# Performance work log

Hardware: AMD Instinct MI355X
Metric: run time of the kernel (lower is better)

The kernel has to match this reference:

```python
import jax, jax.numpy as jnp
import numpy as np

B, N, E, K = 4, 50000, 160000, 1000
C, L = 128, 3


def setup_inputs() -> dict:
    key = jax.random.key(0)
    ks = jax.random.split(key, 16)
    x = jax.random.normal(ks[0], (B, N, 1), jnp.float32)
    edges = jax.random.randint(ks[1], (B, 2, E), 0, N)
    defense_indices = jax.random.randint(ks[2], (B, K), 0, N)
    # GIN layer MLPs: layer l is Linear(in,C) -> ReLU -> Linear(C,C); layer 0 in=1
    w1_first = jax.random.normal(ks[3], (1, C), jnp.float32) * (1.0 / np.sqrt(1))
    w1_rest = jax.random.normal(ks[4], (L - 1, C, C), jnp.float32) * (1.0 / np.sqrt(C))
    w2 = jax.random.normal(ks[5], (L, C, C), jnp.float32) * (1.0 / np.sqrt(C))
    b1 = jax.random.normal(ks[6], (L, C), jnp.float32) * 0.02
    b2 = jax.random.normal(ks[7], (L, C), jnp.float32) * 0.02
    pol_w = jax.random.normal(ks[8], (C, 1), jnp.float32) * (1.0 / np.sqrt(C))
    pol_b = jax.random.normal(ks[9], (1,), jnp.float32) * 0.02
    val_w = jax.random.normal(ks[10], (C, 1), jnp.float32) * (1.0 / np.sqrt(C))
    val_b = jax.random.normal(ks[11], (1,), jnp.float32) * 0.02
    return {"x": x, "edges": edges, "defense_indices": defense_indices,
            "nop_index": 0, "w1_first": w1_first, "w1_rest": w1_rest,
            "w2": w2, "b1": b1, "b2": b2, "pol_w": pol_w, "pol_b": pol_b,
            "val_w": val_w, "val_b": val_b}


def reference(x, edges, defense_indices, nop_index, w1_first, w1_rest, w2, b1, b2, pol_w, pol_b, val_w, val_b):
    def gin_layer(h, src, dst, w1_l, b1_l, w2_l, b2_l):
        # sum-aggregate neighbor features (source_to_target), eps = 0
        agg = jax.ops.segment_sum(h[src], dst, num_segments=N)
        z = h + agg
        return jnp.maximum(z @ w1_l + b1_l, 0.0) @ w2_l + b2_l

    def per_graph(xg, eg):
        src, dst = eg[0], eg[1]
        h = gin_layer(xg, src, dst, w1_first, b1[0], w2[0], b2[0])
        for l in range(1, L):
            h = jnp.maximum(h, 0.0)  # inter-layer activation
            h = gin_layer(h, src, dst, w1_rest[l - 1], b1[l], w2[l], b2[l])
        return h

    emb = jax.vmap(per_graph)(x, edges)       # [B, N, C]
    emb = jnp.maximum(emb, 0.0)               # self.activation after GIN
    def_emb = jax.vmap(lambda e, i: e[i])(emb, defense_indices)  # [B, K, C]
    wait = def_emb[:, nop_index, :]           # [B, C]
    policy = jnp.squeeze(def_emb @ pol_w + pol_b, -1)  # [B, K]
    value = jnp.squeeze(wait @ val_w + val_b)          # [B]
    return (policy, value)
```

## Files before the change

### kernel.cpp

```cpp
#include <hip/hip_runtime.h>
#include <hip/hip_bf16.h>

#define BB 4
#define NN 50000
#define EE 160000
#define KK 1000
#define CH 128
#define TM 64
#define NTILES ((NN + TM - 1) / TM)
#define TILES_TOTAL (BB * NTILES)
#define SCAN_CHUNK 2048
#define SCAN_NB ((NN + SCAN_CHUNK - 1) / SCAN_CHUNK)

typedef unsigned short u16;
typedef unsigned int u32;
typedef __attribute__((ext_vector_type(8))) short short8;
typedef __attribute__((ext_vector_type(4))) float f32x4;

__device__ __forceinline__ int ZIDX(int m, int k) {
  return (m << 7) | (k ^ ((m & 7) << 3));
}

__device__ __forceinline__ u16 f2b(float f) {
  __hip_bfloat16 h = __float2bfloat16(f);
  return *reinterpret_cast<u16*>(&h);
}
__device__ __forceinline__ float b2f(u32 lo16) {
  return __uint_as_float(lo16 << 16);
}

__global__ __launch_bounds__(256)
void prep_all(const float* __restrict__ w1r, const float* __restrict__ w2,
              u16* __restrict__ img, int* __restrict__ cnt) {
  int stride = gridDim.x * blockDim.x;
  int gtid = blockIdx.x * blockDim.x + threadIdx.x;
  for (int i = gtid; i < BB * NN; i += stride) cnt[i] = 0;
  for (int f = gtid; f < 5 * CH * CH; f += stride) {
    int e = f & 7;
    int lane = (f >> 3) & 63;
    int ks = (f >> 9) & 3;
    int ct = (f >> 11) & 1;
    int wv = (f >> 12) & 3;
    int mat = f >> 14;
    int n = wv * 32 + ct * 16 + (lane & 15);
    int k = ks * 32 + (lane >> 4) * 8 + e;
    const float* src;
    switch (mat) {
      case 0: src = w2; break;
      case 1: src = w1r; break;
      case 2: src = w2 + 16384; break;
      case 3: src = w1r + 16384; break;
      default: src = w2 + 32768; break;
    }
    img[f] = f2b(src[(k << 7) + n]);
  }
}

__global__ __launch_bounds__(256)
void csr_count(const int* __restrict__ edges, int* __restrict__ cnt) {
  int stride = gridDim.x * blockDim.x;
  for (int i = blockIdx.x * blockDim.x + threadIdx.x; i < BB * EE; i += stride) {
    int b = i / EE, e = i - b * EE;
    int dst = edges[(b * 2 + 1) * EE + e];
    atomicAdd(&cnt[b * NN + dst], 1);
  }
}

__global__ __launch_bounds__(256)
void scan_local(const int* __restrict__ cnt, int* __restrict__ offs,
                int* __restrict__ bsum) {
  __shared__ int sdata[256];
  const int g = blockIdx.y, blk = blockIdx.x, t = threadIdx.x;
  const int i0 = blk * SCAN_CHUNK + t * 8;
  int v[8];
  int s = 0;
#pragma unroll
  for (int j = 0; j < 8; ++j) {
    int i = i0 + j;
    v[j] = (i < NN) ? cnt[g * NN + i] : 0;
    s += v[j];
  }
  sdata[t] = s;
  __syncthreads();
#pragma unroll
  for (int off = 1; off < 256; off <<= 1) {
    int vv = (t >= off) ? sdata[t - off] : 0;
    __syncthreads();
    sdata[t] += vv;
    __syncthreads();
  }
  int run = sdata[t] - s;
#pragma unroll
  for (int j = 0; j < 8; ++j) {
    int i = i0 + j;
    if (i < NN) offs[g * (NN + 1) + i] = run;
    run += v[j];
  }
  if (t == 255) bsum[g * SCAN_NB + blk] = sdata[255];
}

__global__ __launch_bounds__(256)
void scan_add(int* __restrict__ offs, int* __restrict__ woff,
              const int* __restrict__ bsum) {
  const int g = blockIdx.y, blk = blockIdx.x, t = threadIdx.x;
  int boff = 0;
  for (int j = 0; j < blk; ++j) boff += bsum[g * SCAN_NB + j];
  const int i0 = blk * SCAN_CHUNK + t * 8;
#pragma unroll
  for (int j = 0; j < 8; ++j) {
    int i = i0 + j;
    if (i < NN) {
      int val = offs[g * (NN + 1) + i] + boff;
      offs[g * (NN + 1) + i] = val;
      woff[g * NN + i] = val;
    }
  }
  if (blk == SCAN_NB - 1 && t == 255)
    offs[g * (NN + 1) + NN] = boff + bsum[g * SCAN_NB + blk];
}

__global__ __launch_bounds__(256)
void csr_fill(const int* __restrict__ edges, int* __restrict__ woff,
              int* __restrict__ csr) {
  int stride = gridDim.x * blockDim.x;
  for (int i = blockIdx.x * blockDim.x + threadIdx.x; i < BB * EE; i += stride) {
    int b = i / EE, e = i - b * EE;
    int src = edges[(b * 2) * EE + e];
    int dst = edges[(b * 2 + 1) * EE + e];
    int pos = atomicAdd(&woff[b * NN + dst], 1);
    csr[b * EE + pos] = (src << 6) | (dst & 63);
  }
}

template <bool L0>
__global__ __launch_bounds__(256, 4)
void gin_layer(const void* __restrict__ hin_v, u16* __restrict__ hout,
               const int* __restrict__ offs, const int* __restrict__ csr,
               const float* __restrict__ w1f,
               const u16* __restrict__ imgf_w1,
               const u16* __restrict__ imgf_w2,
               const float* __restrict__ b1v, const float* __restrict__ b2v) {
  __shared__ u16 zt[TM * CH];
  __shared__ float part[TM * 4];

  const int tid = threadIdx.x;
  const int lane = tid & 63;
  const int wv = tid >> 6;
  const int lr = lane & 15;
  const int g = lane >> 4;
  const int cb = wv * 32;

  const int wg = blockIdx.x;
  const int tile = (wg & 7) * (TILES_TOTAL / 8) + (wg >> 3);
  const int b = tile / NTILES;
  const int t0 = (tile % NTILES) * TM;
  const int nm = min(TM, NN - t0);

  const int m = tid >> 2;
  const int p = tid & 3;

  if (L0) {
    const float* x = (const float*)hin_v;
    int start = 0, end = 0;
    if (m < nm) {
      start = offs[b * (NN + 1) + t0 + m];
      end = offs[b * (NN + 1) + t0 + m + 1];
    }
    float s = 0.f;
    if (m < nm) {
      if (p == 0) s = x[b * NN + t0 + m];
      for (int e = start + p; e < end; e += 4)
        s += x[b * NN + (((u32)csr[b * EE + e]) >> 6)];
    }
    part[(m << 2) + p] = s;
    __syncthreads();
    float z0 = part[m << 2] + part[(m << 2) + 1] + part[(m << 2) + 2] +
               part[(m << 2) + 3];
#pragma unroll
    for (int jj = 0; jj < 4; ++jj) {
      int c0 = (p << 5) + (jj << 3);
      short8 tv;
#pragma unroll
      for (int t = 0; t < 8; ++t)
        tv[t] = (short)f2b(fmaxf(z0 * w1f[c0 + t] + b1v[c0 + t], 0.f));
      *(short8*)&zt[ZIDX(m, c0)] = tv;
    }
    __syncthreads();
  } else {
    const u16* h = (const u16*)hin_v;
    int start = 0, end = 0;
    if (m < nm) {
      start = offs[b * (NN + 1) + t0 + m];
      end = offs[b * (NN + 1) + t0 + m + 1];
    }
    float acc[32];
    if (m < nm) {
      const uint4* hr =
          (const uint4*)(h + ((size_t)(b * NN + t0 + m) << 7)) + (p << 2);
#pragma unroll
      for (int j = 0; j < 4; ++j) {
        uint4 v = hr[j];
        acc[j*8+0] = b2f(v.x & 0xffff); acc[j*8+1] = b2f(v.x >> 16);
        acc[j*8+2] = b2f(v.y & 0xffff); acc[j*8+3] = b2f(v.y >> 16);
        acc[j*8+4] = b2f(v.z & 0xffff); acc[j*8+5] = b2f(v.z >> 16);
        acc[j*8+6] = b2f(v.w & 0xffff); acc[j*8+7] = b2f(v.w >> 16);
      }
      for (int e = start; e < end; ++e) {
        int src = ((u32)csr[b * EE + e]) >> 6;
        const uint4* sr =
            (const uint4*)(h + ((size_t)(b * NN + src) << 7)) + (p << 2);
#pragma unroll
        for (int j = 0; j < 4; ++j) {
          uint4 v = sr[j];
          acc[j*8+0] += b2f(v.x & 0xffff); acc[j*8+1] += b2f(v.x >> 16);
          acc[j*8+2] += b2f(v.y & 0xffff); acc[j*8+3] += b2f(v.y >> 16);
          acc[j*8+4] += b2f(v.z & 0xffff); acc[j*8+5] += b2f(v.z >> 16);
          acc[j*8+6] += b2f(v.w & 0xffff); acc[j*8+7] += b2f(v.w >> 16);
        }
      }
    } else {
#pragma unroll
      for (int t = 0; t < 32; ++t) acc[t] = 0.f;
    }
#pragma unroll
    for (int jj = 0; jj < 4; ++jj) {
      int c0 = (p << 5) + (jj << 3);
      short8 tv;
#pragma unroll
      for (int t = 0; t < 8; ++t) tv[t] = (short)f2b(acc[(jj << 3) + t]);
      *(short8*)&zt[ZIDX(m, c0)] = tv;
    }
    __syncthreads();

    short8 fw1[2][4];
#pragma unroll
    for (int ct = 0; ct < 2; ++ct)
#pragma unroll
      for (int ks = 0; ks < 4; ++ks)
        fw1[ct][ks] = *(const short8*)
            &imgf_w1[(((((wv << 1) | ct) << 2) | ks) << 9) + (lane << 3)];
    f32x4 a1[4][2];
#pragma unroll
    for (int rt = 0; rt < 4; ++rt)
#pragma unroll
      for (int ct = 0; ct < 2; ++ct) a1[rt][ct] = (f32x4){0.f, 0.f, 0.f, 0.f};
#pragma unroll
    for (int ks = 0; ks < 4; ++ks) {
      int kb = (ks << 5) + (g << 3);
      short8 af[4];
#pragma unroll
      for (int rt = 0; rt < 4; ++rt)
        af[rt] = *(const short8*)&zt[ZIDX((rt << 4) + lr, kb)];
#pragma unroll
      for (int rt = 0; rt < 4; ++rt)
#pragma unroll
        for (int ct = 0; ct < 2; ++ct)
          a1[rt][ct] = __builtin_amdgcn_mfma_f32_16x16x32_bf16(
              af[rt], fw1[ct][ks], a1[rt][ct], 0, 0, 0);
    }
    __syncthreads();

#pragma unroll
    for (int rt = 0; rt < 4; ++rt)
#pragma unroll
      for (int ct = 0; ct < 2; ++ct) {
        int col = cb + (ct << 4) + lr;
        float bias = b1v[col];
#pragma unroll
        for (int r = 0; r < 4; ++r) {
          int row = (rt << 4) + (g << 2) + r;
          zt[ZIDX(row, col)] = f2b(fmaxf(a1[rt][ct][r] + bias, 0.f));
        }
      }
    __syncthreads();
  }

  short8 fw2[2][4];
#pragma unroll
  for (int ct = 0; ct < 2; ++ct)
#pragma unroll
    for (int ks = 0; ks < 4; ++ks)
      fw2[ct][ks] = *(const short8*)
          &imgf_w2[(((((wv << 1) | ct) << 2) | ks) << 9) + (lane << 3)];
  f32x4 a2[4][2];
#pragma unroll
  for (int rt = 0; rt < 4; ++rt)
#pragma unroll
    for (int ct = 0; ct < 2; ++ct) a2[rt][ct] = (f32x4){0.f, 0.f, 0.f, 0.f};
#pragma unroll
  for (int ks = 0; ks < 4; ++ks) {
    int kb = (ks << 5) + (g << 3);
    short8 af[4];
#pragma unroll
    for (int rt = 0; rt < 4; ++rt)
      af[rt] = *(const short8*)&zt[ZIDX((rt << 4) + lr, kb)];
#pragma unroll
    for (int rt = 0; rt < 4; ++rt)
#pragma unroll
      for (int ct = 0; ct < 2; ++ct)
        a2[rt][ct] = __builtin_amdgcn_mfma_f32_16x16x32_bf16(
            af[rt], fw2[ct][ks], a2[rt][ct], 0, 0, 0);
  }
  __syncthreads();

#pragma unroll
  for (int rt = 0; rt < 4; ++rt)
#pragma unroll
    for (int ct = 0; ct < 2; ++ct) {
      int col = cb + (ct << 4) + lr;
      float bias = b2v[col];
#pragma unroll
      for (int r = 0; r < 4; ++r) {
        int row = (rt << 4) + (g << 2) + r;
        zt[ZIDX(row, col)] = f2b(fmaxf(a2[rt][ct][r] + bias, 0.f));
      }
    }
  __syncthreads();

  for (int i = tid; i < 1024; i += 256) {
    int mm = i >> 4, c0 = (i & 15) << 3;
    if (mm < nm) {
      uint4 v = *(const uint4*)&zt[ZIDX(mm, c0)];
      *(uint4*)&hout[(((size_t)(b * NN + t0 + mm)) << 7) + c0] = v;
    }
  }
}

__global__ __launch_bounds__(256)
void heads_kernel(const u16* __restrict__ emb, const int* __restrict__ didx,
                  const int* __restrict__ nopp, const float* __restrict__ pol_w,
                  const float* __restrict__ pol_b, const float* __restrict__ val_w,
                  const float* __restrict__ val_b, float* __restrict__ out) {
  int gw = (blockIdx.x * blockDim.x + threadIdx.x) >> 6;
  int lane = threadIdx.x & 63;
  if (gw >= BB * KK) return;
  int b = gw / KK, k = gw - b * KK;
  int node = didx[b * KK + k];
  const u16* e = emb + (((size_t)(b * NN + node)) << 7);
  u32 v = *(const u32*)&e[lane << 1];
  float f0 = __uint_as_float(v << 16);
  float f1 = __uint_as_float(v & 0xffff0000u);
  float s = f0 * pol_w[lane << 1] + f1 * pol_w[(lane << 1) + 1];
#pragma unroll
  for (int off = 32; off; off >>= 1) s += __shfl_down(s, off);
  if (lane == 0) out[b * KK + k] = s + pol_b[0];
  if (k == nopp[0]) {
    float vv = f0 * val_w[lane << 1] + f1 * val_w[(lane << 1) + 1];
#pragma unroll
    for (int off = 32; off; off >>= 1) vv += __shfl_down(vv, off);
    if (lane == 0) out[BB * KK + b] = vv + val_b[0];
  }
}

extern "C" void kernel_launch(void* const* d_in, const int* in_sizes, int n_in,
                              void* d_out, int out_size, void* d_ws, size_t ws_size,
                              hipStream_t stream) {
  const float* x     = (const float*)d_in[0];
  const int*   edges = (const int*)d_in[1];
  const int*   didx  = (const int*)d_in[2];
  const int*   nopp  = (const int*)d_in[3];
  const float* w1f   = (const float*)d_in[4];
  const float* w1r   = (const float*)d_in[5];
  const float* w2    = (const float*)d_in[6];
  const float* b1    = (const float*)d_in[7];
  const float* b2    = (const float*)d_in[8];
  const float* pol_w = (const float*)d_in[9];
  const float* pol_b = (const float*)d_in[10];
  const float* val_w = (const float*)d_in[11];
  const float* val_b = (const float*)d_in[12];
  float* out = (float*)d_out;

  char* ws = (char*)d_ws;
  u16* hA = (u16*)ws;            ws += (size_t)BB * NN * CH * 2;
  u16* hB = (u16*)ws;            ws += (size_t)BB * NN * CH * 2;
  u16* img = (u16*)ws;           ws += (size_t)5 * CH * CH * 2;
  int* offs = (int*)ws;          ws += (size_t)BB * (NN + 1) * 4;
  int* woff = (int*)ws;          ws += (size_t)BB * NN * 4;
  int* cnt  = (int*)ws;          ws += (size_t)BB * NN * 4;
  int* bsum = (int*)ws;          ws += (size_t)BB * SCAN_NB * 4;
  int* csr  = (int*)ws;          ws += (size_t)BB * EE * 4;

  prep_all<<<784, 256, 0, stream>>>(w1r, w2, img, cnt);
  csr_count<<<1250, 256, 0, stream>>>(edges, cnt);
  scan_local<<<dim3(SCAN_NB, BB), 256, 0, stream>>>(cnt, offs, bsum);
  scan_add<<<dim3(SCAN_NB, BB), 256, 0, stream>>>(offs, woff, bsum);
  csr_fill<<<1250, 256, 0, stream>>>(edges, woff, csr);

  gin_layer<true><<<TILES_TOTAL, 256, 0, stream>>>(
      x, hA, offs, csr, w1f, nullptr, img, b1, b2);
  gin_layer<false><<<TILES_TOTAL, 256, 0, stream>>>(
      hA, hB, offs, csr, nullptr, img + 1 * 16384, img + 2 * 16384,
      b1 + CH, b2 + CH);
  gin_layer<false><<<TILES_TOTAL, 256, 0, stream>>>(
      hB, hA, offs, csr, nullptr, img + 3 * 16384, img + 4 * 16384,
      b1 + 2 * CH, b2 + 2 * CH);

  heads_kernel<<<(BB * KK * 64 + 255) / 256, 256, 0, stream>>>(
      hA, didx, nopp, pol_w, pol_b, val_w, val_b, out);
}
```

Measured before the change: 290.2 us.

## Sort nodes by in-degree so GIN tiles have balanced neighbor loops

Adds a per-graph counting-sort kernel that orders nodes by in-degree (capped at 63) and makes each GIN layer tile process a permuted set of nodes, gathering and scattering rows through the permutation. The aim is to cut wavefront divergence from uneven per-node edge loops, since threads in a wave then see similar degrees. The cost is an extra small kernel that runs on only 4 blocks, indirect offs/row accesses, and scattered output writes that lose contiguity.

```diff
diff --git a/kernel.cpp b/kernel.cpp
--- a/kernel.cpp
+++ b/kernel.cpp
@@ -128,13 +128,36 @@
     int src = edges[(b * 2) * EE + e];
     int dst = edges[(b * 2 + 1) * EE + e];
     int pos = atomicAdd(&woff[b * NN + dst], 1);
-    csr[b * EE + pos] = (src << 6) | (dst & 63);
+    csr[b * EE + pos] = src;
+  }
+}
+
+__global__ __launch_bounds__(256)
+void sort_nodes(const int* __restrict__ cnt, int* __restrict__ perm) {
+  __shared__ int hist[64];
+  __shared__ int base[64];
+  const int g = blockIdx.x, t = threadIdx.x;
+  if (t < 64) hist[t] = 0;
+  __syncthreads();
+  for (int i = t; i < NN; i += 256)
+    atomicAdd(&hist[min(cnt[g * NN + i], 63)], 1);
+  __syncthreads();
+  if (t == 0) {
+    int run = 0;
+    for (int d = 0; d < 64; ++d) { base[d] = run; run += hist[d]; }
+  }
+  __syncthreads();
+  for (int i = t; i < NN; i += 256) {
+    int d = min(cnt[g * NN + i], 63);
+    int pos = atomicAdd(&base[d], 1);
+    perm[g * NN + pos] = i;
   }
 }
 
 template <bool L0>
 __global__ __launch_bounds__(256, 4)
 void gin_layer(const void* __restrict__ hin_v, u16* __restrict__ hout,
+               const int* __restrict__ perm,
                const int* __restrict__ offs, const int* __restrict__ csr,
                const float* __restrict__ w1f,
                const u16* __restrict__ imgf_w1,
@@ -142,6 +165,7 @@
                const float* __restrict__ b1v, const float* __restrict__ b2v) {
   __shared__ u16 zt[TM * CH];
   __shared__ float part[TM * 4];
+  __shared__ int nid[TM];
 
   const int tid = threadIdx.x;
   const int lane = tid & 63;
@@ -159,18 +183,22 @@
   const int m = tid >> 2;
   const int p = tid & 3;
 
+  if (tid < TM) nid[tid] = (tid < nm) ? perm[b * NN + t0 + tid] : 0;
+  __syncthreads();
+
   if (L0) {
     const float* x = (const float*)hin_v;
+    int node = nid[m];
     int start = 0, end = 0;
     if (m < nm) {
-      start = offs[b * (NN + 1) + t0 + m];
-      end = offs[b * (NN + 1) + t0 + m + 1];
+      start = offs[b * (NN + 1) + node];
+      end = offs[b * (NN + 1) + node + 1];
     }
     float s = 0.f;
     if (m < nm) {
-      if (p == 0) s = x[b * NN + t0 + m];
+      if (p == 0) s = x[b * NN + node];
       for (int e = start + p; e < end; e += 4)
-        s += x[b * NN + (((u32)csr[b * EE + e]) >> 6)];
+        s += x[b * NN + csr[b * EE + e]];
     }
     part[(m << 2) + p] = s;
     __syncthreads();
@@ -188,15 +216,16 @@
     __syncthreads();
   } else {
     const u16* h = (const u16*)hin_v;
+    int node = nid[m];
     int start = 0, end = 0;
     if (m < nm) {
-      start = offs[b * (NN + 1) + t0 + m];
-      end = offs[b * (NN + 1) + t0 + m + 1];
+      start = offs[b * (NN + 1) + node];
+      end = offs[b * (NN + 1) + node + 1];
     }
     float acc[32];
     if (m < nm) {
       const uint4* hr =
-          (const uint4*)(h + ((size_t)(b * NN + t0 + m) << 7)) + (p << 2);
+          (const uint4*)(h + ((size_t)(b * NN + node) << 7)) + (p << 2);
 #pragma unroll
       for (int j = 0; j < 4; ++j) {
         uint4 v = hr[j];
@@ -206,7 +235,7 @@
         acc[j*8+6] = b2f(v.w & 0xffff); acc[j*8+7] = b2f(v.w >> 16);
       }
       for (int e = start; e < end; ++e) {
-        int src = ((u32)csr[b * EE + e]) >> 6;
+        int src = csr[b * EE + e];
         const uint4* sr =
             (const uint4*)(h + ((size_t)(b * NN + src) << 7)) + (p << 2);
 #pragma unroll
@@ -321,7 +350,7 @@
     int mm = i >> 4, c0 = (i & 15) << 3;
     if (mm < nm) {
       uint4 v = *(const uint4*)&zt[ZIDX(mm, c0)];
-      *(uint4*)&hout[(((size_t)(b * NN + t0 + mm)) << 7) + c0] = v;
+      *(uint4*)&hout[(((size_t)(b * NN + nid[mm])) << 7) + c0] = v;
     }
   }
 }
@@ -377,6 +406,7 @@
   int* offs = (int*)ws;          ws += (size_t)BB * (NN + 1) * 4;
   int* woff = (int*)ws;          ws += (size_t)BB * NN * 4;
   int* cnt  = (int*)ws;          ws += (size_t)BB * NN * 4;
+  int* perm = (int*)ws;          ws += (size_t)BB * NN * 4;
   int* bsum = (int*)ws;          ws += (size_t)BB * SCAN_NB * 4;
   int* csr  = (int*)ws;          ws += (size_t)BB * EE * 4;
 
@@ -385,14 +415,15 @@
   scan_local<<<dim3(SCAN_NB, BB), 256, 0, stream>>>(cnt, offs, bsum);
   scan_add<<<dim3(SCAN_NB, BB), 256, 0, stream>>>(offs, woff, bsum);
   csr_fill<<<1250, 256, 0, stream>>>(edges, woff, csr);
+  sort_nodes<<<BB, 256, 0, stream>>>(cnt, perm);
 
   gin_layer<true><<<TILES_TOTAL, 256, 0, stream>>>(
-      x, hA, offs, csr, w1f, nullptr, img, b1, b2);
+      x, hA, perm, offs, csr, w1f, nullptr, img, b1, b2);
   gin_layer<false><<<TILES_TOTAL, 256, 0, stream>>>(
-      hA, hB, offs, csr, nullptr, img + 1 * 16384, img + 2 * 16384,
+      hA, hB, perm, offs, csr, nullptr, img + 1 * 16384, img + 2 * 16384,
       b1 + CH, b2 + CH);
   gin_layer<false><<<TILES_TOTAL, 256, 0, stream>>>(
-      hB, hA, offs, csr, nullptr, img + 3 * 16384, img + 4 * 16384,
+      hB, hA, perm, offs, csr, nullptr, img + 3 * 16384, img + 4 * 16384,
       b1 + 2 * CH, b2 + 2 * CH);
 
   heads_kernel<<<(BB * KK * 64 + 255) / 256, 256, 0, stream>>>(
```

New measurement: 384.1 us. 1.32x slower.
